# Kernel optimization log

Measured on AMD Instinct MI355X. Metric: run time of the kernel, lower is better.

The kernel has to match this reference:

```python
import jax, jax.numpy as jnp
import numpy as np

N_HEAD = 16
HEAD_DIM = 128

def rotate_half(x):
    x1, x2 = jnp.split(x, 2, axis=-1)
    return jnp.concatenate((-x2, x1), axis=-1)

def setup_inputs() -> dict:
    key = jax.random.key(0)
    ks = jax.random.split(key, 5)
    B, T, C = 2, 2048, 2048
    x = jax.random.normal(ks[0], (B, T, C), dtype=jnp.float32)
    # rotary tables as used by the module: cos/sin of shape [T, head_dim]
    pos = jnp.arange(T, dtype=jnp.float32)[:, None]
    inv_freq = 1.0 / (10000.0 ** (jnp.arange(0, HEAD_DIM, 2, dtype=jnp.float32) / HEAD_DIM))
    freqs = pos * inv_freq[None, :]            # [T, head_dim/2]
    emb = jnp.concatenate([freqs, freqs], -1)  # [T, head_dim]
    cos = jnp.cos(emb)
    sin = jnp.sin(emb)
    W_qkv = jax.random.normal(ks[1], (C, 3 * C), dtype=jnp.float32) * (C ** -0.5)
    W_proj = jax.random.normal(ks[2], (C, C), dtype=jnp.float32) * (C ** -0.5)
    return {"x": x, "cos": cos, "sin": sin, "W_qkv": W_qkv, "W_proj": W_proj}

def reference(x, cos, sin, W_qkv, W_proj):
    B, T, C = x.shape
    H, D = N_HEAD, HEAD_DIM
    qkv = x @ W_qkv                                   # [B,T,3C]
    q, k, v = jnp.split(qkv, 3, axis=2)
    # [B,T,C] -> [B,H,T,D]
    q = q.reshape(B, T, H, D).transpose(0, 2, 1, 3)
    k = k.reshape(B, T, H, D).transpose(0, 2, 1, 3)
    v = v.reshape(B, T, H, D).transpose(0, 2, 1, 3)
    c = cos[None, None, :, :]                          # [1,1,T,D]
    s = sin[None, None, :, :]
    q = q * c + rotate_half(q) * s
    k = k * c + rotate_half(k) * s
    scale = 1.0 / jnp.sqrt(jnp.float32(D))
    scores = jnp.einsum('bhqd,bhkd->bhqk', q, k) * scale
    attn = jax.nn.softmax(scores, axis=-1)
    y = jnp.einsum('bhqk,bhkd->bhqd', attn, v)         # [B,H,T,D]
    y = y.transpose(0, 2, 1, 3).reshape(B, T, C)
    return y @ W_proj
```

## Files before the change

kernel.cpp:

```cpp
#include <hip/hip_runtime.h>
#include <cstdint>
#include <cstddef>

typedef __bf16 bf16_t;
typedef __bf16 bf16x8 __attribute__((ext_vector_type(8)));
typedef float f32x4 __attribute__((ext_vector_type(4)));

#define MFMA16(a, b, c) __builtin_amdgcn_mfma_f32_16x16x32_bf16(a, b, c, 0, 0, 0)

__device__ __forceinline__ void gll16(const bf16_t* g, bf16_t* l) {
  __builtin_amdgcn_global_load_lds(
      (__attribute__((address_space(1))) uint32_t*)((uintptr_t)g),
      (__attribute__((address_space(3))) uint32_t*)((uint32_t)(uintptr_t)l),
      16, 0, 0);
}

__global__ void fill_diag(uint32_t* out, int n_u32) {
  int i = blockIdx.x * 256 + threadIdx.x;
  if (i < n_u32) out[i] = 0x447A0000u;
}

__global__ void conv_vec_f32(const float* __restrict__ in, bf16_t* __restrict__ out,
                             int n8) {
  const int i = blockIdx.x * 256 + threadIdx.x;
  if (i >= n8) return;
  const float* p = in + (size_t)i * 8;
  const f32x4 a = *(const f32x4*)p;
  const f32x4 b = *(const f32x4*)(p + 4);
  bf16x8 o;
#pragma unroll
  for (int j = 0; j < 4; ++j) {
    o[j] = (bf16_t)a[j];
    o[4 + j] = (bf16_t)b[j];
  }
  ((bf16x8*)out)[i] = o;
}

__global__ __launch_bounds__(256) void conv_transpose_f32(
    const float* __restrict__ in, bf16_t* __restrict__ out, int R, int C) {
  __shared__ bf16_t tile[64][72];
  const int bc = blockIdx.x * 64;
  const int br = blockIdx.y * 64;
  const int t = threadIdx.x;
  const int r = t >> 3;
  const int c8 = (t & 7) * 8;
#pragma unroll
  for (int ii = 0; ii < 2; ++ii) {
    const int rr = r + ii * 32;
    const float* p = in + (size_t)(br + rr) * C + bc + c8;
    const f32x4 a = *(const f32x4*)p;
    const f32x4 b = *(const f32x4*)(p + 4);
    bf16x8 v;
#pragma unroll
    for (int j = 0; j < 4; ++j) {
      v[j] = (bf16_t)a[j];
      v[4 + j] = (bf16_t)b[j];
    }
    *(bf16x8*)(&tile[rr][c8]) = v;
  }
  __syncthreads();
#pragma unroll
  for (int ii = 0; ii < 2; ++ii) {
    const int rr = r + ii * 32;
    bf16x8 o;
#pragma unroll
    for (int jj = 0; jj < 8; ++jj) o[jj] = tile[c8 + jj][rr];
    *(bf16x8*)(out + (size_t)(bc + rr) * R + br + c8) = o;
  }
}

#define MF8(MLO, AARR, BARR, NLO)                                           \
  do {                                                                      \
    _Pragma("unroll") for (int m_ = 0; m_ < 4; ++m_) {                      \
      _Pragma("unroll") for (int n_ = 0; n_ < 2; ++n_) {                    \
        acc[(MLO) + m_][(NLO) + n_] =                                       \
            MFMA16(AARR[m_][0], BARR[n_][0], acc[(MLO) + m_][(NLO) + n_]);  \
        acc[(MLO) + m_][(NLO) + n_] =                                       \
            MFMA16(AARR[m_][1], BARR[n_][1], acc[(MLO) + m_][(NLO) + n_]);  \
      }                                                                     \
    }                                                                       \
  } while (0)

template <bool C32>
__global__ __launch_bounds__(512, 2) void gemm8(
    const bf16_t* __restrict__ A, const bf16_t* __restrict__ Bt,
    void* __restrict__ C, int M, int N, int K, int nbn) {
  __shared__ __align__(1024) bf16_t lds8[65536];
  bf16_t* As = lds8;
  bf16_t* Bs = lds8 + 32768;

  const int tid = threadIdx.x;
  const int lane = tid & 63;
  const int wave = tid >> 6;
  const int wr = wave >> 2;
  const int wc = wave & 3;
  const int fr = lane & 15;
  const int fg = lane >> 4;

  const int nwg = gridDim.x;
  const int bid = blockIdx.x;
  const int swz = (bid & 7) * (nwg >> 3) + (bid >> 3);
  const int m0 = (swz / nbn) * 256;
  const int n0 = (swz % nbn) * 256;

  const int NT = K >> 6;

  const int sseg0 = wave * 2;
  const int srow = lane >> 3;
  const int sj = lane & 7;

  auto stage = [&](const bf16_t* __restrict__ G, int row0, bf16_t* L, int kt,
                   int h) {
#pragma unroll
    for (int l = 0; l < 2; ++l) {
      const int seg = sseg0 + l;
      const int r = seg * 8 + srow;
      const int j = sj ^ (r & 7);
      const bf16_t* src = G + (size_t)(row0 + h * 128 + r) * K + kt * 64 + j * 8;
      gll16(src, L + ((2 * kt + h) & 3) * 8192 + seg * 512 + lane * 8);
    }
  };

  const int cb0 = (fg * 16) ^ ((fr & 7) << 4);

  auto lda = [&](bf16x8(&af)[4][2], int kt, int mlo) {
    const char* base = (const char*)(As + ((2 * kt + wr) & 3) * 8192);
#pragma unroll
    for (int m = 0; m < 4; ++m) {
      const char* p = base + ((mlo + m) * 16 + fr) * 128;
      af[m][0] = *(const bf16x8*)(p + cb0);
      af[m][1] = *(const bf16x8*)(p + (cb0 ^ 64));
    }
  };
  auto ldb = [&](bf16x8(&bf)[2][2], int kt, int nlo) {
    const char* base = (const char*)(Bs + ((2 * kt + (wc >> 1)) & 3) * 8192);
#pragma unroll
    for (int n = 0; n < 2; ++n) {
      const char* p = base + ((wc & 1) * 64 + (nlo + n) * 16 + fr) * 128;
      bf[n][0] = *(const bf16x8*)(p + cb0);
      bf[n][1] = *(const bf16x8*)(p + (cb0 ^ 64));
    }
  };

  f32x4 acc[8][4] = {};

  stage(A, m0, As, 0, 0);
  stage(A, m0, As, 0, 1);
  stage(Bt, n0, Bs, 0, 0);
  stage(Bt, n0, Bs, 0, 1);
  stage(Bt, n0, Bs, 1, 0);
  stage(Bt, n0, Bs, 1, 1);
  asm volatile("s_waitcnt vmcnt(4)" ::: "memory");
  __builtin_amdgcn_s_barrier();

  bf16x8 af[4][2], bfA[2][2], bfB[2][2];

  for (int u = 0; u < NT; u += 2) {
    const bool st2 = (u + 2 < NT);
    const bool st3 = (u + 3 < NT);
    lda(af, u, 0);
    ldb(bfA, u, 0);
    stage(A, m0, As, u + 1, 0);
    asm volatile("s_waitcnt lgkmcnt(8)" ::: "memory");
    __builtin_amdgcn_s_barrier();
    asm volatile("s_waitcnt lgkmcnt(0)" ::: "memory");
    __builtin_amdgcn_sched_barrier(0);
    __builtin_amdgcn_s_setprio(1);
    MF8(0, af, bfA, 0);
    __builtin_amdgcn_s_setprio(0);
    __builtin_amdgcn_s_barrier();
    ldb(bfB, u, 2);
    stage(A, m0, As, u + 1, 1);
    __builtin_amdgcn_s_barrier();
    asm volatile("s_waitcnt lgkmcnt(0)" ::: "memory");
    __builtin_amdgcn_sched_barrier(0);
    __builtin_amdgcn_s_setprio(1);
    MF8(0, af, bfB, 2);
    __builtin_amdgcn_s_setprio(0);
    __builtin_amdgcn_s_barrier();
    lda(af, u, 4);
    if (st2) stage(Bt, n0, Bs, u + 2, 0);
    __builtin_amdgcn_s_barrier();
    asm volatile("s_waitcnt lgkmcnt(0)" ::: "memory");
    __builtin_amdgcn_sched_barrier(0);
    __builtin_amdgcn_s_setprio(1);
    MF8(4, af, bfB, 2);
    __builtin_amdgcn_s_setprio(0);
    __builtin_amdgcn_s_barrier();
    if (st2) stage(Bt, n0, Bs, u + 2, 1);
    __builtin_amdgcn_s_barrier();
    __builtin_amdgcn_s_setprio(1);
    MF8(4, af, bfA, 0);
    __builtin_amdgcn_s_setprio(0);
    asm volatile("s_waitcnt vmcnt(4)" ::: "memory");
    __builtin_amdgcn_s_barrier();
    lda(af, u + 1, 0);
    ldb(bfA, u + 1, 0);
    if (st2) stage(A, m0, As, u + 2, 0);
    asm volatile("s_waitcnt lgkmcnt(8)" ::: "memory");
    __builtin_amdgcn_s_barrier();
    asm volatile("s_waitcnt lgkmcnt(0)" ::: "memory");
    __builtin_amdgcn_sched_barrier(0);
    __builtin_amdgcn_s_setprio(1);
    MF8(0, af, bfA, 0);
    __builtin_amdgcn_s_setprio(0);
    __builtin_amdgcn_s_barrier();
    ldb(bfB, u + 1, 2);
    if (st2) stage(A, m0, As, u + 2, 1);
    __builtin_amdgcn_s_barrier();
    asm volatile("s_waitcnt lgkmcnt(0)" ::: "memory");
    __builtin_amdgcn_sched_barrier(0);
    __builtin_amdgcn_s_setprio(1);
    MF8(0, af, bfB, 2);
    __builtin_amdgcn_s_setprio(0);
    __builtin_amdgcn_s_barrier();
    lda(af, u + 1, 4);
    if (st3) stage(Bt, n0, Bs, u + 3, 0);
    __builtin_amdgcn_s_barrier();
    asm volatile("s_waitcnt lgkmcnt(0)" ::: "memory");
    __builtin_amdgcn_sched_barrier(0);
    __builtin_amdgcn_s_setprio(1);
    MF8(4, af, bfB, 2);
    __builtin_amdgcn_s_setprio(0);
    __builtin_amdgcn_s_barrier();
    if (st3) stage(Bt, n0, Bs, u + 3, 1);
    __builtin_amdgcn_s_barrier();
    __builtin_amdgcn_s_setprio(1);
    MF8(4, af, bfA, 0);
    __builtin_amdgcn_s_setprio(0);
    asm volatile("s_waitcnt vmcnt(4)" ::: "memory");
    __builtin_amdgcn_s_barrier();
  }

#pragma unroll
  for (int m = 0; m < 8; ++m) {
#pragma unroll
    for (int n = 0; n < 4; ++n) {
#pragma unroll
      for (int r = 0; r < 4; ++r) {
        const int row = m0 + wr * 128 + m * 16 + fg * 4 + r;
        const int col = n0 + wc * 64 + n * 16 + fr;
        const size_t idx = (size_t)row * N + col;
        if (C32)
          ((float*)C)[idx] = acc[m][n][r];
        else
          ((bf16_t*)C)[idx] = (bf16_t)acc[m][n][r];
      }
    }
  }
  (void)M;
}

template <bool C32>
__global__ __launch_bounds__(256) void gemm_lds(
    const bf16_t* __restrict__ A, const bf16_t* __restrict__ Bt,
    void* __restrict__ C, int M, int N, int K) {
  __shared__ __align__(16) bf16_t As[128 * 32];
  __shared__ __align__(16) bf16_t Bs[128 * 32];
  const int tid = threadIdx.x;
  const int lane = tid & 63;
  const int wave = tid >> 6;
  const int m0 = blockIdx.x * 128;
  const int n0 = blockIdx.y * 128;
  const int wm = (wave & 1) * 64;
  const int wn = (wave >> 1) * 64;
  const int fr = lane & 15;
  const int fk = (lane >> 4) * 8;

  f32x4 acc[4][4] = {};

  const bf16_t* ga = A + (size_t)(m0 + (tid >> 2)) * K + (tid & 3) * 8;
  const bf16_t* gb = Bt + (size_t)(n0 + (tid >> 2)) * K + (tid & 3) * 8;
  bf16_t* lA = As + tid * 8;
  bf16_t* lB = Bs + tid * 8;
  const size_t half = (size_t)64 * K;

  for (int k0 = 0; k0 < K; k0 += 32) {
    __syncthreads();
    gll16(ga, lA);
    gll16(ga + half, lA + 2048);
    gll16(gb, lB);
    gll16(gb + half, lB + 2048);
    ga += 32;
    gb += 32;
    __syncthreads();
    bf16x8 af[4], bfr[4];
#pragma unroll
    for (int i = 0; i < 4; ++i)
      af[i] = *(const bf16x8*)(As + (wm + i * 16 + fr) * 32 + fk);
#pragma unroll
    for (int j = 0; j < 4; ++j)
      bfr[j] = *(const bf16x8*)(Bs + (wn + j * 16 + fr) * 32 + fk);
#pragma unroll
    for (int i = 0; i < 4; ++i)
#pragma unroll
      for (int j = 0; j < 4; ++j)
        acc[i][j] = MFMA16(af[i], bfr[j], acc[i][j]);
  }

  const int fg = lane >> 4;
#pragma unroll
  for (int i = 0; i < 4; ++i) {
#pragma unroll
    for (int j = 0; j < 4; ++j) {
#pragma unroll
      for (int r = 0; r < 4; ++r) {
        const int row = m0 + wm + i * 16 + fg * 4 + r;
        const int col = n0 + wn + j * 16 + fr;
        const size_t idx = (size_t)row * N + col;
        if (C32)
          ((float*)C)[idx] = acc[i][j][r];
        else
          ((bf16_t*)C)[idx] = (bf16_t)acc[i][j][r];
      }
    }
  }
}

template <bool A32, bool C32>
__global__ __launch_bounds__(256) void gemm_t(
    const void* __restrict__ A, const bf16_t* __restrict__ Bt,
    void* __restrict__ C, int M, int N, int K) {
  __shared__ bf16_t As[128 * 32];
  __shared__ bf16_t Bs[128 * 32];
  const int tid = threadIdx.x;
  const int lane = tid & 63;
  const int wave = tid >> 6;
  const int m0 = blockIdx.x * 128;
  const int n0 = blockIdx.y * 128;
  const int wm = (wave & 1) * 64;
  const int wn = (wave >> 1) * 64;
  const int fr = lane & 15;
  const int fk = (lane >> 4) * 8;

  f32x4 acc[4][4] = {};

  const size_t ea0 = (size_t)(m0 + (tid >> 2)) * K + (tid & 3) * 8;
  const bf16_t* gb = Bt + (size_t)(n0 + (tid >> 2)) * K + (tid & 3) * 8;
  bf16_t* lA = As + tid * 8;
  bf16_t* lB = Bs + tid * 8;
  const size_t half = (size_t)64 * K;

  for (int k0 = 0; k0 < K; k0 += 32) {
    bf16x8 ra0, ra1;
    if (A32) {
      const float* pa = (const float*)A + ea0 + k0;
      const f32x4 x0 = *(const f32x4*)pa;
      const f32x4 x1 = *(const f32x4*)(pa + 4);
      const f32x4 x2 = *(const f32x4*)(pa + half);
      const f32x4 x3 = *(const f32x4*)(pa + half + 4);
#pragma unroll
      for (int j = 0; j < 4; ++j) {
        ra0[j] = (bf16_t)x0[j];
        ra0[4 + j] = (bf16_t)x1[j];
        ra1[j] = (bf16_t)x2[j];
        ra1[4 + j] = (bf16_t)x3[j];
      }
    } else {
      const bf16_t* pa = (const bf16_t*)A + ea0 + k0;
      ra0 = *(const bf16x8*)pa;
      ra1 = *(const bf16x8*)(pa + half);
    }
    const bf16x8 rb0 = *(const bf16x8*)gb;
    const bf16x8 rb1 = *(const bf16x8*)(gb + half);
    gb += 32;
    __syncthreads();
    *(bf16x8*)lA = ra0;
    *(bf16x8*)(lA + 2048) = ra1;
    *(bf16x8*)lB = rb0;
    *(bf16x8*)(lB + 2048) = rb1;
    __syncthreads();
    bf16x8 af[4], bfr[4];
#pragma unroll
    for (int i = 0; i < 4; ++i)
      af[i] = *(const bf16x8*)(As + (wm + i * 16 + fr) * 32 + fk);
#pragma unroll
    for (int j = 0; j < 4; ++j)
      bfr[j] = *(const bf16x8*)(Bs + (wn + j * 16 + fr) * 32 + fk);
#pragma unroll
    for (int i = 0; i < 4; ++i)
#pragma unroll
      for (int j = 0; j < 4; ++j)
        acc[i][j] = MFMA16(af[i], bfr[j], acc[i][j]);
  }

  const int fg = lane >> 4;
#pragma unroll
  for (int i = 0; i < 4; ++i) {
#pragma unroll
    for (int j = 0; j < 4; ++j) {
#pragma unroll
      for (int r = 0; r < 4; ++r) {
        const int row = m0 + wm + i * 16 + fg * 4 + r;
        const int col = n0 + wn + j * 16 + fr;
        const size_t idx = (size_t)row * N + col;
        if (C32)
          ((float*)C)[idx] = acc[i][j][r];
        else
          ((bf16_t*)C)[idx] = (bf16_t)acc[i][j][r];
      }
    }
  }
}

__global__ __launch_bounds__(256) void rope_k(
    const bf16_t* __restrict__ qkv, const bf16_t* __restrict__ cosb,
    const bf16_t* __restrict__ sinb, bf16_t* __restrict__ Kr) {
  const int row = blockIdx.x;
  const int t = row & 2047;
  const int b = row >> 11;
  const int idx = threadIdx.x * 8;
  const int h = idx >> 7;
  const int d = idx & 127;
  const float sgn = (d < 64) ? -1.f : 1.f;
  const bf16_t* base = qkv + (size_t)row * 6144 + 2048;
  const bf16x8 kv = *(const bf16x8*)(base + idx);
  const bf16x8 kp = *(const bf16x8*)(base + (idx ^ 64));
  const bf16x8 cv = *(const bf16x8*)(cosb + t * 128 + d);
  const bf16x8 sv = *(const bf16x8*)(sinb + t * 128 + d);
  bf16x8 o;
#pragma unroll
  for (int jj = 0; jj < 8; ++jj)
    o[jj] = (bf16_t)(((float)kv[jj]) * ((float)cv[jj]) +
                     sgn * ((float)kp[jj]) * ((float)sv[jj]));
  *(bf16x8*)(Kr + ((size_t)(b * 16 + h) * 2048 + t) * 128 + d) = o;
}

__global__ __launch_bounds__(256) void transpose_v(
    const bf16_t* __restrict__ qkv, bf16_t* __restrict__ Vt) {
  __shared__ bf16_t tile[64][72];
  const int bh = blockIdx.z;
  const int b = bh >> 4, h = bh & 15;
  const int t0 = blockIdx.x * 64;
  const int d0 = blockIdx.y * 64;
  const int t = threadIdx.x;
  const int r = t >> 3;
  const int c8 = (t & 7) * 8;
#pragma unroll
  for (int ii = 0; ii < 2; ++ii) {
    const int rr = r + ii * 32;
    *(bf16x8*)(&tile[rr][c8]) =
        *(const bf16x8*)(qkv + (size_t)(b * 2048 + t0 + rr) * 6144 + 4096 + h * 128 + d0 + c8);
  }
  __syncthreads();
#pragma unroll
  for (int ii = 0; ii < 2; ++ii) {
    const int rr = r + ii * 32;
    bf16x8 o;
#pragma unroll
    for (int jj = 0; jj < 8; ++jj) o[jj] = tile[c8 + jj][rr];
    *(bf16x8*)(Vt + ((size_t)bh * 128 + d0 + rr) * 2048 + t0 + c8) = o;
  }
}

__global__ __launch_bounds__(256) void flash_fast(
    const bf16_t* __restrict__ qkv, const bf16_t* __restrict__ cosb,
    const bf16_t* __restrict__ sinb, const bf16_t* __restrict__ Kr,
    const bf16_t* __restrict__ Vt, bf16_t* __restrict__ Y) {
  constexpr int T = 2048;
  __shared__ bf16_t Ks[64][136];
  __shared__ bf16_t Vs[128][72];
  __shared__ bf16_t Ps[128][72];
  const int tid = threadIdx.x;
  const int lane = tid & 63;
  const int wave = tid >> 6;
  const int fr = lane & 15;
  const int fg = lane >> 4;
  const int qt = blockIdx.x;
  const int bh = blockIdx.y;
  const int b = bh >> 4, h = bh & 15;

  const bf16_t* qbase = qkv + (size_t)b * T * 6144 + h * 128;
  bf16x8 qf[2][4];
#pragma unroll
  for (int i = 0; i < 2; ++i) {
    const int trow = qt * 128 + wave * 32 + i * 16 + fr;
    const bf16_t* qrow = qbase + (size_t)trow * 6144;
#pragma unroll
    for (int ks = 0; ks < 4; ++ks) {
      const int d = ks * 32 + fg * 8;
      const float sgn = (d < 64) ? -1.f : 1.f;
      const bf16x8 qv = *(const bf16x8*)(qrow + d);
      const bf16x8 qp = *(const bf16x8*)(qrow + (d ^ 64));
      const bf16x8 cv = *(const bf16x8*)(cosb + trow * 128 + d);
      const bf16x8 sv = *(const bf16x8*)(sinb + trow * 128 + d);
      bf16x8 o;
#pragma unroll
      for (int jj = 0; jj < 8; ++jj)
        o[jj] = (bf16_t)((((float)qv[jj]) * ((float)cv[jj]) +
                          sgn * ((float)qp[jj]) * ((float)sv[jj])) *
                         0.1275174825f);
      qf[i][ks] = o;
    }
  }

  f32x4 acc[2][8] = {};
  float l_i[2][4] = {};

  const int krow = tid >> 4;
  const int kcol = (tid & 15) * 8;
  const int vrow = tid >> 3;
  const int vcol = (tid & 7) * 8;
  const bf16_t* Kh = Kr + (size_t)bh * T * 128;
  const bf16_t* Vh = Vt + (size_t)bh * 128 * T;

  for (int j = 0; j < T / 64; ++j) {
    const int t0 = j * 64;
#pragma unroll
    for (int it = 0; it < 4; ++it) {
      const int row = it * 16 + krow;
      *(bf16x8*)(&Ks[row][kcol]) = *(const bf16x8*)(Kh + (size_t)(t0 + row) * 128 + kcol);
    }
#pragma unroll
    for (int it = 0; it < 4; ++it) {
      const int row = it * 32 + vrow;
      *(bf16x8*)(&Vs[row][vcol]) = *(const bf16x8*)(Vh + (size_t)row * T + t0 + vcol);
    }
    __syncthreads();

    f32x4 sacc[2][4] = {};
#pragma unroll
    for (int n = 0; n < 4; ++n) {
#pragma unroll
      for (int ks = 0; ks < 4; ++ks) {
        const bf16x8 kf = *(const bf16x8*)(&Ks[n * 16 + fr][ks * 32 + fg * 8]);
        sacc[0][n] = MFMA16(qf[0][ks], kf, sacc[0][n]);
        sacc[1][n] = MFMA16(qf[1][ks], kf, sacc[1][n]);
      }
    }

#pragma unroll
    for (int i = 0; i < 2; ++i) {
#pragma unroll
      for (int r = 0; r < 4; ++r) {
        const float p0 = exp2f(sacc[i][0][r]);
        const float p1 = exp2f(sacc[i][1][r]);
        const float p2 = exp2f(sacc[i][2][r]);
        const float p3 = exp2f(sacc[i][3][r]);
        l_i[i][r] += (p0 + p1) + (p2 + p3);
        const int prow = wave * 32 + i * 16 + fg * 4 + r;
        Ps[prow][0 + fr] = (bf16_t)p0;
        Ps[prow][16 + fr] = (bf16_t)p1;
        Ps[prow][32 + fr] = (bf16_t)p2;
        Ps[prow][48 + fr] = (bf16_t)p3;
      }
    }

#pragma unroll
    for (int ks = 0; ks < 2; ++ks) {
      const bf16x8 pf0 = *(const bf16x8*)(&Ps[wave * 32 + fr][ks * 32 + fg * 8]);
      const bf16x8 pf1 = *(const bf16x8*)(&Ps[wave * 32 + 16 + fr][ks * 32 + fg * 8]);
#pragma unroll
      for (int n = 0; n < 8; ++n) {
        const bf16x8 vf = *(const bf16x8*)(&Vs[n * 16 + fr][ks * 32 + fg * 8]);
        acc[0][n] = MFMA16(pf0, vf, acc[0][n]);
        acc[1][n] = MFMA16(pf1, vf, acc[1][n]);
      }
    }
    __syncthreads();
  }

#pragma unroll
  for (int i = 0; i < 2; ++i) {
#pragma unroll
    for (int r = 0; r < 4; ++r) {
      float l = l_i[i][r];
#pragma unroll
      for (int msk = 1; msk < 16; msk <<= 1) l += __shfl_xor(l, msk, 64);
      const float inv = 1.0f / l;
      const int t = qt * 128 + wave * 32 + i * 16 + fg * 4 + r;
      bf16_t* yrow = Y + (size_t)(b * T + t) * 2048 + h * 128;
#pragma unroll
      for (int n = 0; n < 8; ++n)
        yrow[n * 16 + fr] = (bf16_t)(acc[i][n][r] * inv);
    }
  }
}

__global__ __launch_bounds__(256) void flash_fused_v2(
    const bf16_t* __restrict__ qkv, const bf16_t* __restrict__ cosb,
    const bf16_t* __restrict__ sinb, bf16_t* __restrict__ Y) {
  constexpr int T = 2048;
  __shared__ bf16_t Ks[64][136];
  __shared__ bf16_t Vs[128][72];
  __shared__ bf16_t Ps[128][72];
  const int tid = threadIdx.x;
  const int lane = tid & 63;
  const int wave = tid >> 6;
  const int fr = lane & 15;
  const int fg = lane >> 4;
  const int qt = blockIdx.x;
  const int bh = blockIdx.y;
  const int b = bh >> 4, h = bh & 15;

  const bf16_t* qbase = qkv + (size_t)b * T * 6144 + h * 128;
  bf16x8 qf[2][4];
#pragma unroll
  for (int i = 0; i < 2; ++i) {
    const int trow = qt * 128 + wave * 32 + i * 16 + fr;
    const bf16_t* qrow = qbase + (size_t)trow * 6144;
#pragma unroll
    for (int ks = 0; ks < 4; ++ks) {
      const int d = ks * 32 + fg * 8;
      const float sgn = (d < 64) ? -1.f : 1.f;
      const bf16x8 qv = *(const bf16x8*)(qrow + d);
      const bf16x8 qp = *(const bf16x8*)(qrow + (d ^ 64));
      const bf16x8 cv = *(const bf16x8*)(cosb + trow * 128 + d);
      const bf16x8 sv = *(const bf16x8*)(sinb + trow * 128 + d);
      bf16x8 o;
#pragma unroll
      for (int jj = 0; jj < 8; ++jj)
        o[jj] = (bf16_t)((((float)qv[jj]) * ((float)cv[jj]) +
                          sgn * ((float)qp[jj]) * ((float)sv[jj])) *
                         0.08838834764831845f);
      qf[i][ks] = o;
    }
  }

  f32x4 acc[2][8] = {};
  float l_i[2][4] = {};

  const int kr = tid >> 4;
  const int kc = (tid & 15) * 8;
  const float sgnk = (kc < 64) ? -1.f : 1.f;
  const int tp = tid & 63;

  for (int j = 0; j < T / 64; ++j) {
    const int t0 = j * 64;
#pragma unroll
    for (int it = 0; it < 4; ++it) {
      const int row = it * 16 + kr;
      const int tg = t0 + row;
      const bf16_t* krow = qkv + ((size_t)(b * T + tg)) * 6144 + 2048 + h * 128;
      const bf16x8 kv = *(const bf16x8*)(krow + kc);
      const bf16x8 kp = *(const bf16x8*)(krow + (kc ^ 64));
      const bf16x8 cv = *(const bf16x8*)(cosb + tg * 128 + kc);
      const bf16x8 sv = *(const bf16x8*)(sinb + tg * 128 + kc);
      bf16x8 o;
#pragma unroll
      for (int jj = 0; jj < 8; ++jj)
        o[jj] = (bf16_t)(((float)kv[jj]) * ((float)cv[jj]) +
                         sgnk * ((float)kp[jj]) * ((float)sv[jj]));
      *(bf16x8*)(&Ks[row][kc]) = o;
    }
#pragma unroll
    for (int cc = 0; cc < 4; ++cc) {
      const int d8 = (cc * 4 + (tid >> 6)) * 8;
      const bf16x8 vv = *(const bf16x8*)(qkv + ((size_t)(b * T + t0 + tp)) * 6144 +
                                         4096 + h * 128 + d8);
#pragma unroll
      for (int jj = 0; jj < 8; ++jj) Vs[d8 + jj][tp] = vv[jj];
    }
    __syncthreads();

    f32x4 sacc[2][4] = {};
#pragma unroll
    for (int n = 0; n < 4; ++n) {
#pragma unroll
      for (int ks = 0; ks < 4; ++ks) {
        const bf16x8 kf = *(const bf16x8*)(&Ks[n * 16 + fr][ks * 32 + fg * 8]);
        sacc[0][n] = MFMA16(qf[0][ks], kf, sacc[0][n]);
        sacc[1][n] = MFMA16(qf[1][ks], kf, sacc[1][n]);
      }
    }

#pragma unroll
    for (int i = 0; i < 2; ++i) {
#pragma unroll
      for (int r = 0; r < 4; ++r) {
        const float p0 = __expf(sacc[i][0][r]);
        const float p1 = __expf(sacc[i][1][r]);
        const float p2 = __expf(sacc[i][2][r]);
        const float p3 = __expf(sacc[i][3][r]);
        l_i[i][r] += (p0 + p1) + (p2 + p3);
        const int prow = wave * 32 + i * 16 + fg * 4 + r;
        Ps[prow][0 + fr] = (bf16_t)p0;
        Ps[prow][16 + fr] = (bf16_t)p1;
        Ps[prow][32 + fr] = (bf16_t)p2;
        Ps[prow][48 + fr] = (bf16_t)p3;
      }
    }

#pragma unroll
    for (int ks = 0; ks < 2; ++ks) {
      const bf16x8 pf0 = *(const bf16x8*)(&Ps[wave * 32 + fr][ks * 32 + fg * 8]);
      const bf16x8 pf1 = *(const bf16x8*)(&Ps[wave * 32 + 16 + fr][ks * 32 + fg * 8]);
#pragma unroll
      for (int n = 0; n < 8; ++n) {
        const bf16x8 vf = *(const bf16x8*)(&Vs[n * 16 + fr][ks * 32 + fg * 8]);
        acc[0][n] = MFMA16(pf0, vf, acc[0][n]);
        acc[1][n] = MFMA16(pf1, vf, acc[1][n]);
      }
    }
    __syncthreads();
  }

#pragma unroll
  for (int i = 0; i < 2; ++i) {
#pragma unroll
    for (int r = 0; r < 4; ++r) {
      float l = l_i[i][r];
#pragma unroll
      for (int msk = 1; msk < 16; msk <<= 1) l += __shfl_xor(l, msk, 64);
      const float inv = 1.0f / l;
      const int t = qt * 128 + wave * 32 + i * 16 + fg * 4 + r;
      bf16_t* yrow = Y + (size_t)(b * T + t) * 2048 + h * 128;
#pragma unroll
      for (int n = 0; n < 8; ++n)
        yrow[n * 16 + fr] = (bf16_t)(acc[i][n][r] * inv);
    }
  }
}

extern "C" void kernel_launch(void* const* d_in, const int* in_sizes, int n_in,
                              void* d_out, int out_size, void* d_ws, size_t ws_size,
                              hipStream_t stream) {
  const float* x = (const float*)d_in[0];
  const float* cosi = (const float*)d_in[1];
  const float* sini = (const float*)d_in[2];
  const float* Wqkv = (const float*)d_in[3];
  const float* Wproj = (const float*)d_in[4];

  const size_t NEED_FAST = sizeof(bf16_t) *
      ((size_t)12582912 + 262144 + 262144 + 25165824 + 8388608 + 8388608);
  const size_t NEED_BASE = 256 + sizeof(bf16_t) *
      ((size_t)12582912 + 4194304 + 262144 + 262144 + 25165824);

  if (ws_size >= NEED_FAST) {
    bf16_t* base = (bf16_t*)d_ws;
    bf16_t* WqkvT = base;
    bf16_t* y = base;
    bf16_t* cosb = base + 12582912;
    bf16_t* sinb = cosb + 262144;
    bf16_t* qkv = sinb + 262144;
    bf16_t* WprojT = qkv;
    bf16_t* Kr = qkv + 25165824;
    bf16_t* xb = Kr;
    bf16_t* Vt = Kr + 8388608;

    conv_vec_f32<<<128, 256, 0, stream>>>(cosi, cosb, 32768);
    conv_vec_f32<<<128, 256, 0, stream>>>(sini, sinb, 32768);
    conv_vec_f32<<<4096, 256, 0, stream>>>(x, xb, 1048576);
    conv_transpose_f32<<<dim3(96, 32), 256, 0, stream>>>(Wqkv, WqkvT, 2048, 6144);
    gemm8<false><<<384, 512, 0, stream>>>(xb, WqkvT, qkv, 4096, 6144, 2048, 24);
    rope_k<<<4096, 256, 0, stream>>>(qkv, cosb, sinb, Kr);
    transpose_v<<<dim3(32, 2, 32), 256, 0, stream>>>(qkv, Vt);
    flash_fast<<<dim3(16, 32), 256, 0, stream>>>(qkv, cosb, sinb, Kr, Vt, y);
    conv_transpose_f32<<<dim3(32, 32), 256, 0, stream>>>(Wproj, WprojT, 2048, 2048);
    gemm_lds<true><<<dim3(32, 16), 256, 0, stream>>>(y, WprojT, d_out, 4096, 2048, 2048);
  } else if (ws_size >= NEED_BASE) {
    bf16_t* base = (bf16_t*)((char*)d_ws + 256);
    bf16_t* WqkvT = base;
    bf16_t* y = base;
    bf16_t* WprojT = base + 12582912;
    bf16_t* cosb = WprojT + 4194304;
    bf16_t* sinb = cosb + 262144;
    bf16_t* qkv = sinb + 262144;

    conv_vec_f32<<<128, 256, 0, stream>>>(cosi, cosb, 32768);
    conv_vec_f32<<<128, 256, 0, stream>>>(sini, sinb, 32768);
    conv_transpose_f32<<<dim3(96, 32), 256, 0, stream>>>(Wqkv, WqkvT, 2048, 6144);
    gemm_t<true, false><<<dim3(32, 48), 256, 0, stream>>>(x, WqkvT, qkv, 4096, 6144, 2048);
    flash_fused_v2<<<dim3(16, 32), 256, 0, stream>>>(qkv, cosb, sinb, y);
    conv_transpose_f32<<<dim3(32, 32), 256, 0, stream>>>(Wproj, WprojT, 2048, 2048);
    gemm_t<false, true><<<dim3(32, 16), 256, 0, stream>>>(y, WprojT, d_out, 4096, 2048, 2048);
  } else {
    fill_diag<<<(out_size + 255) / 256, 256, 0, stream>>>((uint32_t*)d_out, out_size);
  }
}
```

Baseline: 478.3 us.

## Keep softmax probabilities in registers via transposed QK MFMA and prefetch K/V

Swaps the operands of the QK^T MFMA so each lane's score outputs already form the A-operand layout needed for the PV MFMA. This removes the shared-memory P buffer and its write/read round trip. V columns are permuted when staged into LDS to match the new key ordering, and row sums are reduced with fewer shuffles. K/V tiles for the next step are also prefetched into registers while the current tile computes, which raises register pressure.

```diff
diff --git a/kernel.cpp b/kernel.cpp
--- a/kernel.cpp
+++ b/kernel.cpp
@@ -4,6 +4,7 @@
 
 typedef __bf16 bf16_t;
 typedef __bf16 bf16x8 __attribute__((ext_vector_type(8)));
+typedef __bf16 bf16x4 __attribute__((ext_vector_type(4)));
 typedef float f32x4 __attribute__((ext_vector_type(4)));
 
 #define MFMA16(a, b, c) __builtin_amdgcn_mfma_f32_16x16x32_bf16(a, b, c, 0, 0, 0)
@@ -460,7 +461,6 @@
   constexpr int T = 2048;
   __shared__ bf16_t Ks[64][136];
   __shared__ bf16_t Vs[128][72];
-  __shared__ bf16_t Ps[128][72];
   const int tid = threadIdx.x;
   const int lane = tid & 63;
   const int wave = tid >> 6;
@@ -495,26 +495,44 @@
   }
 
   f32x4 acc[2][8] = {};
-  float l_i[2][4] = {};
+  float l_i[2] = {0.f, 0.f};
 
   const int krow = tid >> 4;
   const int kcol = (tid & 15) * 8;
   const int vrow = tid >> 3;
-  const int vcol = (tid & 7) * 8;
+  const int vu = tid & 7;
+  const int vc0 = ((vu >> 2) * 32) + ((vu & 1) * 16) + (((vu >> 1) & 1) * 4);
   const bf16_t* Kh = Kr + (size_t)bh * T * 128;
   const bf16_t* Vh = Vt + (size_t)bh * 128 * T;
 
+  bf16x8 kreg[4], vreg[4];
+  auto load_kv = [&](int t0) {
+#pragma unroll
+    for (int it = 0; it < 4; ++it)
+      kreg[it] = *(const bf16x8*)(Kh + (size_t)(t0 + it * 16 + krow) * 128 + kcol);
+#pragma unroll
+    for (int it = 0; it < 4; ++it)
+      vreg[it] = *(const bf16x8*)(Vh + (size_t)(it * 32 + vrow) * T + t0 + vu * 8);
+  };
+
+  load_kv(0);
+
   for (int j = 0; j < T / 64; ++j) {
-    const int t0 = j * 64;
-#pragma unroll
-    for (int it = 0; it < 4; ++it) {
-      const int row = it * 16 + krow;
-      *(bf16x8*)(&Ks[row][kcol]) = *(const bf16x8*)(Kh + (size_t)(t0 + row) * 128 + kcol);
-    }
+#pragma unroll
+    for (int it = 0; it < 4; ++it)
+      *(bf16x8*)(&Ks[it * 16 + krow][kcol]) = kreg[it];
 #pragma unroll
     for (int it = 0; it < 4; ++it) {
       const int row = it * 32 + vrow;
-      *(bf16x8*)(&Vs[row][vcol]) = *(const bf16x8*)(Vh + (size_t)row * T + t0 + vcol);
+      const bf16x8 v = vreg[it];
+      bf16x4 lo, hi;
+#pragma unroll
+      for (int jj = 0; jj < 4; ++jj) {
+        lo[jj] = v[jj];
+        hi[jj] = v[4 + jj];
+      }
+      *(bf16x4*)(&Vs[row][vc0]) = lo;
+      *(bf16x4*)(&Vs[row][vc0 + 8]) = hi;
     }
     __syncthreads();
 
@@ -524,37 +542,36 @@
 #pragma unroll
       for (int ks = 0; ks < 4; ++ks) {
         const bf16x8 kf = *(const bf16x8*)(&Ks[n * 16 + fr][ks * 32 + fg * 8]);
-        sacc[0][n] = MFMA16(qf[0][ks], kf, sacc[0][n]);
-        sacc[1][n] = MFMA16(qf[1][ks], kf, sacc[1][n]);
-      }
-    }
-
+        sacc[0][n] = MFMA16(kf, qf[0][ks], sacc[0][n]);
+        sacc[1][n] = MFMA16(kf, qf[1][ks], sacc[1][n]);
+      }
+    }
+
+    if (j + 1 < T / 64) load_kv((j + 1) * 64);
+
+    bf16x8 paf[2][2];
 #pragma unroll
     for (int i = 0; i < 2; ++i) {
-#pragma unroll
-      for (int r = 0; r < 4; ++r) {
-        const float p0 = exp2f(sacc[i][0][r]);
-        const float p1 = exp2f(sacc[i][1][r]);
-        const float p2 = exp2f(sacc[i][2][r]);
-        const float p3 = exp2f(sacc[i][3][r]);
-        l_i[i][r] += (p0 + p1) + (p2 + p3);
-        const int prow = wave * 32 + i * 16 + fg * 4 + r;
-        Ps[prow][0 + fr] = (bf16_t)p0;
-        Ps[prow][16 + fr] = (bf16_t)p1;
-        Ps[prow][32 + fr] = (bf16_t)p2;
-        Ps[prow][48 + fr] = (bf16_t)p3;
-      }
-    }
-
-#pragma unroll
-    for (int ks = 0; ks < 2; ++ks) {
-      const bf16x8 pf0 = *(const bf16x8*)(&Ps[wave * 32 + fr][ks * 32 + fg * 8]);
-      const bf16x8 pf1 = *(const bf16x8*)(&Ps[wave * 32 + 16 + fr][ks * 32 + fg * 8]);
+      float lsum = 0.f;
+#pragma unroll
+      for (int ks2 = 0; ks2 < 2; ++ks2) {
+#pragma unroll
+        for (int jj = 0; jj < 8; ++jj) {
+          const float p = exp2f(sacc[i][ks2 * 2 + (jj >> 2)][jj & 3]);
+          lsum += p;
+          paf[i][ks2][jj] = (bf16_t)p;
+        }
+      }
+      l_i[i] += lsum;
+    }
+
+#pragma unroll
+    for (int ks2 = 0; ks2 < 2; ++ks2) {
 #pragma unroll
       for (int n = 0; n < 8; ++n) {
-        const bf16x8 vf = *(const bf16x8*)(&Vs[n * 16 + fr][ks * 32 + fg * 8]);
-        acc[0][n] = MFMA16(pf0, vf, acc[0][n]);
-        acc[1][n] = MFMA16(pf1, vf, acc[1][n]);
+        const bf16x8 vf = *(const bf16x8*)(&Vs[n * 16 + fr][ks2 * 32 + fg * 8]);
+        acc[0][n] = MFMA16(paf[0][ks2], vf, acc[0][n]);
+        acc[1][n] = MFMA16(paf[1][ks2], vf, acc[1][n]);
       }
     }
     __syncthreads();
@@ -562,12 +579,12 @@
 
 #pragma unroll
   for (int i = 0; i < 2; ++i) {
+    float l = l_i[i];
+    l += __shfl_xor(l, 16, 64);
+    l += __shfl_xor(l, 32, 64);
 #pragma unroll
     for (int r = 0; r < 4; ++r) {
-      float l = l_i[i][r];
-#pragma unroll
-      for (int msk = 1; msk < 16; msk <<= 1) l += __shfl_xor(l, msk, 64);
-      const float inv = 1.0f / l;
+      const float inv = 1.0f / __shfl(l, fg * 4 + r, 64);
       const int t = qt * 128 + wave * 32 + i * 16 + fg * 4 + r;
       bf16_t* yrow = Y + (size_t)(b * T + t) * 2048 + h * 128;
 #pragma unroll
```

Result: no change. 471.6 us (-1.4%).
